# Kernel optimization log

Measured on AMD Instinct MI355X. Metric: run time of the kernel, lower is better.

The kernel has to match this reference:

```python
import jax, jax.numpy as jnp
import numpy as np

N_NODES = 50000
N_FEAT = 128
N_RAND_EDGES = 800000
EPS = 1e-12


def _att_edge_weights(x, row, col, n_node):
    """GNNGuard att_coef: per-edge cosine sim, threshold, zero diagonal,
    row-wise L1 normalize, self-loop weight 1/(deg+1), then exp."""
    # cosine similarity per edge via normalized features (avoids NxN matrix)
    norms = jnp.sqrt(jnp.sum(x * x, axis=1, keepdims=True))
    xn = x / jnp.maximum(norms, EPS)
    sim = jnp.sum(xn[row] * xn[col], axis=1)          # [E]
    sim = jnp.where(sim < 0.1, 0.0, sim)              # threshold
    is_self = (row == col)
    sim = jnp.where(is_self, 0.0, sim)                # remove diagonal (self-sim==1)
    # row-wise L1 normalization (sim >= 0 after threshold)
    rowsum = jax.ops.segment_sum(sim, row, num_segments=n_node)
    rs = rowsum[row]
    sim_norm = jnp.where(rs > 0, sim / jnp.where(rs > 0, rs, 1.0), 0.0)
    # degree = number of nonzero normalized entries per row
    deg = jax.ops.segment_sum((sim_norm != 0).astype(sim.dtype), row,
                              num_segments=n_node)
    lam = 1.0 / (deg + 1.0)                           # self-loop gating weight
    w = jnp.where(is_self, lam[row], sim_norm)
    return jnp.exp(w)


def _gcn_conv(x, row, col, edge_weight, W, b, n_node):
    """GCNConv: h = XW; symmetric-normalized weighted aggregation + bias."""
    h = x @ W                                          # [N, out]
    deg = jax.ops.segment_sum(edge_weight, col, num_segments=n_node)
    dinv = jnp.where(deg > 0, jax.lax.rsqrt(jnp.where(deg > 0, deg, 1.0)), 0.0)
    norm = dinv[row] * edge_weight * dinv[col]         # [E]
    out = jax.ops.segment_sum(norm[:, None] * h[row], col, num_segments=n_node)
    return out + b


def setup_inputs() -> dict:
    key = jax.random.key(0)
    ks = jax.random.split(key, 10)
    x = jax.random.normal(ks[0], (N_NODES, N_FEAT), dtype=jnp.float32)
    # random edges with no self-loops, then append all self-loops
    row = jax.random.randint(ks[1], (N_RAND_EDGES,), 0, N_NODES, dtype=jnp.int32)
    off = jax.random.randint(ks[2], (N_RAND_EDGES,), 1, N_NODES, dtype=jnp.int32)
    col = (row + off) % N_NODES
    loops = jnp.arange(N_NODES, dtype=jnp.int32)
    edge_index = jnp.stack([jnp.concatenate([row, loops]),
                            jnp.concatenate([col, loops])], axis=0)
    s = 1.0 / np.sqrt(N_FEAT)
    W0 = jax.random.normal(ks[3], (N_FEAT, 128), dtype=jnp.float32) * s
    b0 = jnp.zeros((128,), dtype=jnp.float32)
    W1 = jax.random.normal(ks[4], (128, 128), dtype=jnp.float32) * s
    b1 = jnp.zeros((128,), dtype=jnp.float32)
    W2 = jax.random.normal(ks[5], (128, 40), dtype=jnp.float32) * s
    b2 = jnp.zeros((40,), dtype=jnp.float32)
    gate = jax.random.uniform(ks[6], (2,), dtype=jnp.float32)
    return {"x": x, "gate": gate, "W0": W0, "b0": b0, "W1": W1, "b1": b1,
            "W2": W2, "b2": b2, "edge_index": edge_index}


def reference(x, gate, W0, b0, W1, b1, W2, b2, edge_index):
    n = x.shape[0]
    row, col = edge_index[0], edge_index[1]
    Ws = [(W0, b0), (W1, b1), (W2, b2)]
    # layer 0: attention adj from raw features (kept as base adj for gating)
    adj_vals = _att_edge_weights(x, row, col, n)
    h = _gcn_conv(x, row, col, adj_vals, W0, b0, n)
    h = jax.nn.relu(h)
    for i in range(1, 3):
        e_new = _att_edge_weights(h, row, col, n)
        g = gate[i - 1]
        w = g * adj_vals + (1.0 - g) * e_new
        h = _gcn_conv(h, row, col, w, Ws[i][0], Ws[i][1], n)
        if i != 2:
            h = jax.nn.relu(h)
    return jax.nn.log_softmax(h, axis=1)
```

## Files before the change

kernel.cpp:

```cpp
#include <hip/hip_runtime.h>
#include <hip/hip_bf16.h>
#include <math.h>

#define F 128

typedef __attribute__((ext_vector_type(8))) unsigned short ushort8v;

__device__ __forceinline__ float bfu(unsigned short u) {
  return __uint_as_float(((unsigned)u) << 16);
}

__global__ void k_normalize(const float* __restrict__ x, float* __restrict__ xn,
                            __hip_bfloat16* __restrict__ xnb, int N) {
  int wid = (blockIdx.x * blockDim.x + threadIdx.x) >> 6;
  int lane = threadIdx.x & 63;
  if (wid >= N) return;
  const float2* src = (const float2*)(x + (size_t)wid * F);
  float2 v = src[lane];
  float ss = v.x * v.x + v.y * v.y;
#pragma unroll
  for (int m = 32; m >= 1; m >>= 1) ss += __shfl_xor(ss, m);
  float inv = 1.0f / fmaxf(sqrtf(ss), 1e-12f);
  float2 o; o.x = v.x * inv; o.y = v.y * inv;
  ((float2*)(xn + (size_t)wid * F))[lane] = o;
  __hip_bfloat162 ob;
  ob.x = __float2bfloat16(o.x); ob.y = __float2bfloat16(o.y);
  ((__hip_bfloat162*)(xnb + (size_t)wid * F))[lane] = ob;
}

__global__ void k_hist2(const int* __restrict__ row, const int* __restrict__ col,
                        int* __restrict__ cntBoth, int N, int E) {
  int e = blockIdx.x * blockDim.x + threadIdx.x;
  if (e < E) { atomicAdd(cntBoth + col[e], 1); atomicAdd(cntBoth + N + row[e], 1); }
}

__global__ void k_scan1(const int* __restrict__ cnt, int* __restrict__ partial,
                        int* __restrict__ bsum, int M) {
  __shared__ int sm[256];
  int t = threadIdx.x;
  int i = blockIdx.x * 256 + t;
  int val = (i < M) ? cnt[i] : 0;
  sm[t] = val;
  __syncthreads();
  for (int off = 1; off < 256; off <<= 1) {
    int v = (t >= off) ? sm[t - off] : 0;
    __syncthreads();
    sm[t] += v;
    __syncthreads();
  }
  if (i < M) partial[i] = sm[t] - val;
  if (t == 255) bsum[blockIdx.x] = sm[255];
}

__global__ void k_scan2(const int* __restrict__ bsum, int* __restrict__ boffs, int nb) {
  __shared__ int sm[256];
  int t = threadIdx.x;
  int carry = 0;
  for (int base = 0; base < nb; base += 256) {
    int idx = base + t;
    int val = (idx < nb) ? bsum[idx] : 0;
    sm[t] = val;
    __syncthreads();
    for (int off = 1; off < 256; off <<= 1) {
      int v = (t >= off) ? sm[t - off] : 0;
      __syncthreads();
      sm[t] += v;
      __syncthreads();
    }
    if (idx < nb) boffs[idx] = sm[t] - val + carry;
    carry += sm[255];
    __syncthreads();
  }
}

__global__ void k_scan3(const int* __restrict__ partial, const int* __restrict__ boffs,
                        int* __restrict__ offs_c, int* __restrict__ offs_r,
                        int N, int E) {
  int i = blockIdx.x * 256 + threadIdx.x;
  if (i < 2 * N) {
    int v = partial[i] + boffs[i >> 8];
    if (i < N) offs_c[i] = v;
    else offs_r[i - N] = v - E;
  }
  if (i == 0) { offs_c[N] = E; offs_r[N] = E; }
}

__global__ void k_scatter_row(const int* __restrict__ row, const int* __restrict__ offs_r,
                              int* __restrict__ cur_r, int* __restrict__ perm_r, int E) {
  int e = blockIdx.x * blockDim.x + threadIdx.x;
  if (e >= E) return;
  int r = row[e];
  int pos = offs_r[r] + atomicAdd(cur_r + r, 1);
  perm_r[pos] = e;
}

__global__ void k_scatter_col(const int* __restrict__ perm_r, const int* __restrict__ row,
                              const int* __restrict__ col, const int* __restrict__ offs_c,
                              int* __restrict__ cur_c, int* __restrict__ colof_r,
                              int2* __restrict__ pstat, int E) {
  int rp = blockIdx.x * blockDim.x + threadIdx.x;
  if (rp >= E) return;
  int e = perm_r[rp];
  int c = col[e];
  colof_r[rp] = c;
  int pos = offs_c[c] + atomicAdd(cur_c + c, 1);
  int2 rec; rec.x = row[e]; rec.y = rp;
  pstat[pos] = rec;
}

__global__ __launch_bounds__(128) void k_simw(
    const float* __restrict__ xn, const __hip_bfloat16* __restrict__ xnb,
    const int* __restrict__ colof_r, const int* __restrict__ offs_r,
    float* __restrict__ adjr, float* __restrict__ wgr, float* __restrict__ colw,
    const float* __restrict__ gate, int layer) {
  int r = blockIdx.x;
  int t = threadIdx.x;
  int p0 = offs_r[r], p1 = offs_r[r + 1];
  int ne = p1 - p0;
  __shared__ float xr[128];
  __shared__ float sims[320];
  __shared__ int scol[320];
  __shared__ float redv[2];
  __shared__ int redc[2];
  xr[t] = xn[(size_t)r * F + t];
  __syncthreads();
  int g = t >> 4, l = t & 15;
  float4 a0 = *(const float4*)(xr + l * 8);
  float4 a1 = *(const float4*)(xr + l * 8 + 4);
  for (int i = g; i < ne; i += 8) {
    int c = colof_r[p0 + i];
    ushort8v bv = *(const ushort8v*)(xnb + (size_t)c * F + l * 8);
    float s = a0.x * bfu(bv[0]) + a0.y * bfu(bv[1]) + a0.z * bfu(bv[2]) + a0.w * bfu(bv[3])
            + a1.x * bfu(bv[4]) + a1.y * bfu(bv[5]) + a1.z * bfu(bv[6]) + a1.w * bfu(bv[7]);
#pragma unroll
    for (int m = 8; m >= 1; m >>= 1) s += __shfl_xor(s, m);
    bool self = (r == c);
    if (!self && fabsf(s - 0.1f) < 0.02f) {
      const float4* bp = (const float4*)(xn + (size_t)c * F);
      float4 b0 = bp[l * 2], b1 = bp[l * 2 + 1];
      float s2 = a0.x * b0.x + a0.y * b0.y + a0.z * b0.z + a0.w * b0.w
               + a1.x * b1.x + a1.y * b1.y + a1.z * b1.z + a1.w * b1.w;
#pragma unroll
      for (int m = 8; m >= 1; m >>= 1) s2 += __shfl_xor(s2, m);
      s = s2;
    }
    if (l == 0) {
      if (s < 0.1f || self) s = 0.0f;
      sims[i] = s;
      scol[i] = c;
    }
  }
  __syncthreads();
  float v = 0.f; int cn = 0;
  for (int i = t; i < ne; i += 128) {
    float s = sims[i];
    v += s;
    cn += (s > 0.f) ? 1 : 0;
  }
#pragma unroll
  for (int m = 32; m >= 1; m >>= 1) { v += __shfl_xor(v, m); cn += __shfl_xor(cn, m); }
  if ((t & 63) == 0) { redv[t >> 6] = v; redc[t >> 6] = cn; }
  __syncthreads();
  float rs = redv[0] + redv[1];
  int deg = redc[0] + redc[1];
  float lam = 1.0f / (float)(deg + 1);
  float gg = (layer > 0) ? gate[layer - 1] : 0.f;
  for (int i = t; i < ne; i += 128) {
    int c = scol[i];
    float s = sims[i];
    float sn = (rs > 0.f) ? s / rs : 0.f;
    float w = (r == c) ? lam : sn;
    w = expf(w);
    float wc;
    if (layer == 0) { adjr[p0 + i] = w; wc = w; }
    else { wc = gg * adjr[p0 + i] + (1.f - gg) * w; }
    wgr[p0 + i] = wc;
    atomicAdd(colw + c, wc);
  }
}

__global__ __launch_bounds__(256) void k_gemm128(const float* __restrict__ A,
                                                 const float* __restrict__ W,
                                                 __hip_bfloat16* __restrict__ out, int M) {
  __shared__ float As[128][36];
  int t = threadIdx.x;
  int n0 = blockIdx.x * 32;
  for (int i = t; i < 32 * 128; i += 256) {
    int nn = i >> 7, kk = i & 127;
    int gn = n0 + nn;
    As[kk][nn] = (gn < M) ? A[(size_t)gn * 128 + kk] : 0.f;
  }
  __syncthreads();
  int nb = (t >> 6) * 8;
  int j2 = (t & 63) * 2;
  float acc[8][2] = {};
  for (int k = 0; k < 128; ++k) {
    float4 a01 = *(const float4*)&As[k][nb];
    float4 a23 = *(const float4*)&As[k][nb + 4];
    float2 wv = *(const float2*)&W[k * 128 + j2];
    acc[0][0] += a01.x * wv.x; acc[0][1] += a01.x * wv.y;
    acc[1][0] += a01.y * wv.x; acc[1][1] += a01.y * wv.y;
    acc[2][0] += a01.z * wv.x; acc[2][1] += a01.z * wv.y;
    acc[3][0] += a01.w * wv.x; acc[3][1] += a01.w * wv.y;
    acc[4][0] += a23.x * wv.x; acc[4][1] += a23.x * wv.y;
    acc[5][0] += a23.y * wv.x; acc[5][1] += a23.y * wv.y;
    acc[6][0] += a23.z * wv.x; acc[6][1] += a23.z * wv.y;
    acc[7][0] += a23.w * wv.x; acc[7][1] += a23.w * wv.y;
  }
  __hip_bfloat162* o2 = (__hip_bfloat162*)out;
#pragma unroll
  for (int i = 0; i < 8; ++i) {
    int gn = n0 + nb + i;
    if (gn < M) {
      __hip_bfloat162 o;
      o.x = __float2bfloat16(acc[i][0]); o.y = __float2bfloat16(acc[i][1]);
      o2[(size_t)gn * 64 + (j2 >> 1)] = o;
    }
  }
}

__global__ __launch_bounds__(320) void k_gemm40(const float* __restrict__ A,
                                                const float* __restrict__ W,
                                                __hip_bfloat16* __restrict__ out,
                                                int M, int C) {
  __shared__ float As[128][68];
  int t = threadIdx.x;
  int n0 = blockIdx.x * 64;
  for (int i = t; i < 64 * 128; i += 320) {
    int nn = i >> 7, kk = i & 127;
    int gn = n0 + nn;
    As[kk][nn] = (gn < M) ? A[(size_t)gn * 128 + kk] : 0.f;
  }
  __syncthreads();
  int gq = t / 40;
  int jc = t - gq * 40;
  int nb = gq * 8;
  float acc[8] = {};
  for (int k = 0; k < 128; ++k) {
    float4 a01 = *(const float4*)&As[k][nb];
    float4 a23 = *(const float4*)&As[k][nb + 4];
    float wv = W[k * C + jc];
    acc[0] += a01.x * wv; acc[1] += a01.y * wv; acc[2] += a01.z * wv; acc[3] += a01.w * wv;
    acc[4] += a23.x * wv; acc[5] += a23.y * wv; acc[6] += a23.z * wv; acc[7] += a23.w * wv;
  }
#pragma unroll
  for (int i = 0; i < 8; ++i) {
    int gn = n0 + nb + i;
    if (gn < M) out[(size_t)gn * C + jc] = __float2bfloat16(acc[i]);
  }
}

__global__ __launch_bounds__(256) void k_agg_norm(
    const __hip_bfloat162* __restrict__ hWb, const int2* __restrict__ pstat,
    const float* __restrict__ wgr, const float* __restrict__ colw,
    const int* __restrict__ offs_c, const float* __restrict__ bias,
    float* __restrict__ out, float* __restrict__ xn, __hip_bfloat16* __restrict__ xnb,
    int N) {
  int w = threadIdx.x >> 6;
  int t = threadIdx.x & 63;
  int c = blockIdx.x * 4 + w;
  if (c >= N) return;
  int p0 = offs_c[c], p1 = offs_c[c + 1];
  float dcv = colw[c];
  float dic = (dcv > 0.f) ? rsqrtf(dcv) : 0.f;
  float acc0 = bias[2 * t], acc1 = bias[2 * t + 1];
  int p = p0;
  for (; p + 4 <= p1; p += 4) {
    int2 s0 = pstat[p], s1 = pstat[p + 1], s2 = pstat[p + 2], s3 = pstat[p + 3];
    float w0 = wgr[s0.y], w1 = wgr[s1.y], w2 = wgr[s2.y], w3 = wgr[s3.y];
    float d0 = colw[s0.x], d1 = colw[s1.x], d2 = colw[s2.x], d3 = colw[s3.x];
    __hip_bfloat162 h0 = hWb[(size_t)s0.x * 64 + t];
    __hip_bfloat162 h1 = hWb[(size_t)s1.x * 64 + t];
    __hip_bfloat162 h2 = hWb[(size_t)s2.x * 64 + t];
    __hip_bfloat162 h3 = hWb[(size_t)s3.x * 64 + t];
    float n0 = ((d0 > 0.f) ? rsqrtf(d0) : 0.f) * w0 * dic;
    float n1 = ((d1 > 0.f) ? rsqrtf(d1) : 0.f) * w1 * dic;
    float n2 = ((d2 > 0.f) ? rsqrtf(d2) : 0.f) * w2 * dic;
    float n3 = ((d3 > 0.f) ? rsqrtf(d3) : 0.f) * w3 * dic;
    acc0 += n0 * __bfloat162float(h0.x) + n1 * __bfloat162float(h1.x)
          + n2 * __bfloat162float(h2.x) + n3 * __bfloat162float(h3.x);
    acc1 += n0 * __bfloat162float(h0.y) + n1 * __bfloat162float(h1.y)
          + n2 * __bfloat162float(h2.y) + n3 * __bfloat162float(h3.y);
  }
  for (; p < p1; ++p) {
    int2 s0 = pstat[p];
    float w0 = wgr[s0.y];
    float d0 = colw[s0.x];
    __hip_bfloat162 h0 = hWb[(size_t)s0.x * 64 + t];
    float n0 = ((d0 > 0.f) ? rsqrtf(d0) : 0.f) * w0 * dic;
    acc0 += n0 * __bfloat162float(h0.x);
    acc1 += n0 * __bfloat162float(h0.y);
  }
  acc0 = fmaxf(acc0, 0.f); acc1 = fmaxf(acc1, 0.f);
  float2 o; o.x = acc0; o.y = acc1;
  ((float2*)out)[(size_t)c * 64 + t] = o;
  float ss = acc0 * acc0 + acc1 * acc1;
#pragma unroll
  for (int m = 32; m >= 1; m >>= 1) ss += __shfl_xor(ss, m);
  float inv = 1.0f / fmaxf(sqrtf(ss), 1e-12f);
  float2 on; on.x = acc0 * inv; on.y = acc1 * inv;
  ((float2*)xn)[(size_t)c * 64 + t] = on;
  __hip_bfloat162 ob;
  ob.x = __float2bfloat16(on.x); ob.y = __float2bfloat16(on.y);
  ((__hip_bfloat162*)xnb)[(size_t)c * 64 + t] = ob;
}

__global__ __launch_bounds__(256) void k_agg40_lsm(
    const __hip_bfloat16* __restrict__ hW, const int2* __restrict__ pstat,
    const float* __restrict__ wgr, const float* __restrict__ colw,
    const int* __restrict__ offs_c, const float* __restrict__ bias,
    float* __restrict__ out, int C, int N) {
  int w = threadIdx.x >> 6;
  int j = threadIdx.x & 63;
  int c = blockIdx.x * 4 + w;
  if (c >= N) return;
  int p0 = offs_c[c], p1 = offs_c[c + 1];
  float dcv = colw[c];
  float dic = (dcv > 0.f) ? rsqrtf(dcv) : 0.f;
  bool act = j < C;
  int jj = act ? j : 0;
  float acc = act ? bias[jj] : 0.f;
  int p = p0;
  for (; p + 4 <= p1; p += 4) {
    int2 s0 = pstat[p], s1 = pstat[p + 1], s2 = pstat[p + 2], s3 = pstat[p + 3];
    float w0 = wgr[s0.y], w1 = wgr[s1.y], w2 = wgr[s2.y], w3 = wgr[s3.y];
    float d0 = colw[s0.x], d1 = colw[s1.x], d2 = colw[s2.x], d3 = colw[s3.x];
    float h0 = __bfloat162float(hW[(size_t)s0.x * C + jj]);
    float h1 = __bfloat162float(hW[(size_t)s1.x * C + jj]);
    float h2 = __bfloat162float(hW[(size_t)s2.x * C + jj]);
    float h3 = __bfloat162float(hW[(size_t)s3.x * C + jj]);
    acc += ((d0 > 0.f) ? rsqrtf(d0) : 0.f) * w0 * dic * h0
         + ((d1 > 0.f) ? rsqrtf(d1) : 0.f) * w1 * dic * h1
         + ((d2 > 0.f) ? rsqrtf(d2) : 0.f) * w2 * dic * h2
         + ((d3 > 0.f) ? rsqrtf(d3) : 0.f) * w3 * dic * h3;
  }
  for (; p < p1; ++p) {
    int2 s0 = pstat[p];
    float w0 = wgr[s0.y];
    float d0 = colw[s0.x];
    acc += ((d0 > 0.f) ? rsqrtf(d0) : 0.f) * w0 * dic
         * __bfloat162float(hW[(size_t)s0.x * C + jj]);
  }
  if (!act) acc = 0.f;
  float v = act ? acc : -3.0e38f;
#pragma unroll
  for (int m = 32; m >= 1; m >>= 1) v = fmaxf(v, __shfl_xor(v, m));
  float ex = act ? expf(acc - v) : 0.f;
#pragma unroll
  for (int m = 32; m >= 1; m >>= 1) ex += __shfl_xor(ex, m);
  if (act) out[(size_t)c * C + j] = acc - v - logf(ex);
}

extern "C" void kernel_launch(void* const* d_in, const int* in_sizes, int n_in,
                              void* d_out, int out_size, void* d_ws, size_t ws_size,
                              hipStream_t stream) {
  const float* x    = (const float*)d_in[0];
  const float* gate = (const float*)d_in[1];
  const float* W0   = (const float*)d_in[2];
  const float* b0   = (const float*)d_in[3];
  const float* W1   = (const float*)d_in[4];
  const float* b1   = (const float*)d_in[5];
  const float* W2   = (const float*)d_in[6];
  const float* b2   = (const float*)d_in[7];
  const int* eidx   = (const int*)d_in[8];
  int N = in_sizes[0] / 128;
  int E = in_sizes[8] / 2;
  int C = in_sizes[7];
  const int* row = eidx;
  const int* col = eidx + E;

  char* ws = (char*)d_ws;
  size_t off = 0;
  auto alloc = [&](size_t bytes) {
    char* p = ws + off;
    off += (bytes + 255) & ~(size_t)255;
    return p;
  };
  float* xn     = (float*)alloc((size_t)N * 128 * 4);
  __hip_bfloat16* xnb = (__hip_bfloat16*)alloc((size_t)N * 128 * 2);
  float* bufC   = (float*)alloc((size_t)N * 128 * 4);
  __hip_bfloat16* hWb = (__hip_bfloat16*)alloc((size_t)N * 128 * 2);
  float* adjr   = (float*)alloc((size_t)E * 4);
  float* wgr    = (float*)alloc((size_t)E * 4);
  int*   perm_r = (int*)alloc((size_t)E * 4);
  int2*  pstat  = (int2*)alloc((size_t)E * 8);
  int*   colof_r= (int*)alloc((size_t)E * 4);
  int*   offs_c = (int*)alloc((size_t)(N + 1) * 4);
  int*   offs_r = (int*)alloc((size_t)(N + 1) * 4);
  int*   cntB   = (int*)alloc((size_t)N * 4 * 4);
  int*   curB   = cntB + 2 * N;
  int*   partial= (int*)alloc((size_t)N * 4 * 2);
  int*   bsum   = (int*)alloc(2048);
  int*   boffs  = (int*)alloc(2048);
  float* colw   = (float*)alloc((size_t)N * 4);

  int eb  = (E + 255) / 256;
  int nb2 = (2 * N + 255) / 256;
  int nw4 = (N + 3) / 4;

  hipMemsetAsync(cntB, 0, (size_t)N * 4 * 4, stream);
  k_hist2<<<eb, 256, 0, stream>>>(row, col, cntB, N, E);
  k_scan1<<<nb2, 256, 0, stream>>>(cntB, partial, bsum, 2 * N);
  k_scan2<<<1, 256, 0, stream>>>(bsum, boffs, nb2);
  k_scan3<<<nb2, 256, 0, stream>>>(partial, boffs, offs_c, offs_r, N, E);
  k_scatter_row<<<eb, 256, 0, stream>>>(row, offs_r, curB + N, perm_r, E);
  k_scatter_col<<<eb, 256, 0, stream>>>(perm_r, row, col, offs_c, curB,
                                        colof_r, pstat, E);

  for (int layer = 0; layer < 3; ++layer) {
    hipMemsetAsync(colw, 0, (size_t)N * 4, stream);
    if (layer == 0) k_normalize<<<(N + 3) / 4, 256, 0, stream>>>(x, xn, xnb, N);
    k_simw<<<N, 128, 0, stream>>>(xn, xnb, colof_r, offs_r, adjr, wgr, colw, gate, layer);
    const float* hin = (layer == 0) ? x : bufC;
    if (layer < 2) {
      const float* W = (layer == 0) ? W0 : W1;
      const float* b = (layer == 0) ? b0 : b1;
      k_gemm128<<<(N + 31) / 32, 256, 0, stream>>>(hin, W, hWb, N);
      k_agg_norm<<<nw4, 256, 0, stream>>>((const __hip_bfloat162*)hWb, pstat, wgr, colw,
                                          offs_c, b, bufC, xn, xnb, N);
    } else {
      k_gemm40<<<(N + 63) / 64, 320, 0, stream>>>(hin, W2, hWb, N, C);
      k_agg40_lsm<<<nw4, 256, 0, stream>>>(hWb, pstat, wgr, colw, offs_c, b2,
                                           (float*)d_out, C, N);
    }
  }
}
```

Measured before the change: 714.6 us.

## Compute per-edge cosine similarities with MFMA, one wavefront per row

The similarity kernel now gives each row to one wavefront, four rows per block, instead of one 128-thread block per row. Each neighbour's bf16 dot product against the row vector is computed with 16x16x32 bf16 MFMA instructions. The fp32 recheck for similarities near the 0.1 threshold becomes a ballot-driven loop across the whole wave, with the window widened slightly. This aims to cut block-launch and __syncthreads overhead and the scalar dot-product work. In exchange, the MFMA computes a full 16x16 tile when only one column is used, and the threshold fallback is now serialized per wave.

Result: faster. 700.0 us (-2.0%).

```diff
diff --git a/kernel.cpp b/kernel.cpp
--- a/kernel.cpp
+++ b/kernel.cpp
@@ -4,11 +4,8 @@
 
 #define F 128
 
-typedef __attribute__((ext_vector_type(8))) unsigned short ushort8v;
-
-__device__ __forceinline__ float bfu(unsigned short u) {
-  return __uint_as_float(((unsigned)u) << 16);
-}
+typedef __attribute__((ext_vector_type(8))) short bf16x8;
+typedef __attribute__((ext_vector_type(4))) float f32x4;
 
 __global__ void k_normalize(const float* __restrict__ x, float* __restrict__ xn,
                             __hip_bfloat16* __restrict__ xnb, int N) {
@@ -108,72 +105,91 @@
   pstat[pos] = rec;
 }
 
-__global__ __launch_bounds__(128) void k_simw(
+__global__ __launch_bounds__(256) void k_simw(
     const float* __restrict__ xn, const __hip_bfloat16* __restrict__ xnb,
     const int* __restrict__ colof_r, const int* __restrict__ offs_r,
     float* __restrict__ adjr, float* __restrict__ wgr, float* __restrict__ colw,
-    const float* __restrict__ gate, int layer) {
-  int r = blockIdx.x;
-  int t = threadIdx.x;
+    const float* __restrict__ gate, int layer, int N) {
+  int w = threadIdx.x >> 6;
+  int l = threadIdx.x & 63;
+  int r = blockIdx.x * 4 + w;
+  __shared__ float sims[4][320];
+  __shared__ int scol[4][320];
+  if (r >= N) return;
   int p0 = offs_r[r], p1 = offs_r[r + 1];
   int ne = p1 - p0;
-  __shared__ float xr[128];
-  __shared__ float sims[320];
-  __shared__ int scol[320];
-  __shared__ float redv[2];
-  __shared__ int redc[2];
-  xr[t] = xn[(size_t)r * F + t];
-  __syncthreads();
-  int g = t >> 4, l = t & 15;
-  float4 a0 = *(const float4*)(xr + l * 8);
-  float4 a1 = *(const float4*)(xr + l * 8 + 4);
-  for (int i = g; i < ne; i += 8) {
-    int c = colof_r[p0 + i];
-    ushort8v bv = *(const ushort8v*)(xnb + (size_t)c * F + l * 8);
-    float s = a0.x * bfu(bv[0]) + a0.y * bfu(bv[1]) + a0.z * bfu(bv[2]) + a0.w * bfu(bv[3])
-            + a1.x * bfu(bv[4]) + a1.y * bfu(bv[5]) + a1.z * bfu(bv[6]) + a1.w * bfu(bv[7]);
-#pragma unroll
-    for (int m = 8; m >= 1; m >>= 1) s += __shfl_xor(s, m);
-    bool self = (r == c);
-    if (!self && fabsf(s - 0.1f) < 0.02f) {
-      const float4* bp = (const float4*)(xn + (size_t)c * F);
-      float4 b0 = bp[l * 2], b1 = bp[l * 2 + 1];
-      float s2 = a0.x * b0.x + a0.y * b0.y + a0.z * b0.z + a0.w * b0.w
-               + a1.x * b1.x + a1.y * b1.y + a1.z * b1.z + a1.w * b1.w;
-#pragma unroll
-      for (int m = 8; m >= 1; m >>= 1) s2 += __shfl_xor(s2, m);
-      s = s2;
+  int quad = l >> 4;
+  int m = l & 15;
+  int qoff = quad * 8;
+  const __hip_bfloat16* xr = xnb + (size_t)r * F;
+  bf16x8 b0 = *(const bf16x8*)(xr + 0 * 32 + qoff);
+  bf16x8 b1 = *(const bf16x8*)(xr + 1 * 32 + qoff);
+  bf16x8 b2 = *(const bf16x8*)(xr + 2 * 32 + qoff);
+  bf16x8 b3 = *(const bf16x8*)(xr + 3 * 32 + qoff);
+  for (int tb = 0; tb < ne; tb += 16) {
+    int ii = tb + m; if (ii > ne - 1) ii = ne - 1;
+    int cm = colof_r[p0 + ii];
+    if (quad == 0 && tb + m < ne) scol[w][tb + m] = cm;
+    const __hip_bfloat16* xc = xnb + (size_t)cm * F;
+    bf16x8 a0 = *(const bf16x8*)(xc + 0 * 32 + qoff);
+    bf16x8 a1 = *(const bf16x8*)(xc + 1 * 32 + qoff);
+    bf16x8 a2 = *(const bf16x8*)(xc + 2 * 32 + qoff);
+    bf16x8 a3 = *(const bf16x8*)(xc + 3 * 32 + qoff);
+    f32x4 acc = {0.f, 0.f, 0.f, 0.f};
+    acc = __builtin_amdgcn_mfma_f32_16x16x32_bf16(a0, b0, acc, 0, 0, 0);
+    acc = __builtin_amdgcn_mfma_f32_16x16x32_bf16(a1, b1, acc, 0, 0, 0);
+    acc = __builtin_amdgcn_mfma_f32_16x16x32_bf16(a2, b2, acc, 0, 0, 0);
+    acc = __builtin_amdgcn_mfma_f32_16x16x32_bf16(a3, b3, acc, 0, 0, 0);
+    if (m == 0) {
+#pragma unroll
+      for (int reg = 0; reg < 4; ++reg) {
+        int i = tb + quad * 4 + reg;
+        if (i < ne) sims[w][i] = acc[reg];
+      }
     }
-    if (l == 0) {
-      if (s < 0.1f || self) s = 0.0f;
-      sims[i] = s;
-      scol[i] = c;
+  }
+  float vsum = 0.f; int cn = 0;
+  for (int base = 0; base < ne; base += 64) {
+    int i = base + l;
+    bool have = i < ne;
+    float s = have ? sims[w][i] : 0.f;
+    int c = have ? scol[w][i] : r;
+    bool self = (c == r);
+    bool flag = have && !self && fabsf(s - 0.1f) < 0.03f;
+    unsigned long long mask = __ballot(flag);
+    while (mask) {
+      int src = __ffsll(mask) - 1;
+      mask &= mask - 1;
+      int cc = __shfl(c, src);
+      float2 ar = ((const float2*)(xn + (size_t)r * F))[l];
+      float2 bc = ((const float2*)(xn + (size_t)cc * F))[l];
+      float d = ar.x * bc.x + ar.y * bc.y;
+#pragma unroll
+      for (int mm = 32; mm >= 1; mm >>= 1) d += __shfl_xor(d, mm);
+      if (l == src) s = d;
     }
-  }
-  __syncthreads();
-  float v = 0.f; int cn = 0;
-  for (int i = t; i < ne; i += 128) {
-    float s = sims[i];
-    v += s;
+    if (self || s < 0.1f) s = 0.f;
+    if (have) sims[w][i] = s;
+    vsum += s;
     cn += (s > 0.f) ? 1 : 0;
   }
 #pragma unroll
-  for (int m = 32; m >= 1; m >>= 1) { v += __shfl_xor(v, m); cn += __shfl_xor(cn, m); }
-  if ((t & 63) == 0) { redv[t >> 6] = v; redc[t >> 6] = cn; }
-  __syncthreads();
-  float rs = redv[0] + redv[1];
-  int deg = redc[0] + redc[1];
-  float lam = 1.0f / (float)(deg + 1);
+  for (int mm = 32; mm >= 1; mm >>= 1) {
+    vsum += __shfl_xor(vsum, mm);
+    cn += __shfl_xor(cn, mm);
+  }
+  float rs = vsum;
+  float lam = 1.0f / (float)(cn + 1);
   float gg = (layer > 0) ? gate[layer - 1] : 0.f;
-  for (int i = t; i < ne; i += 128) {
-    int c = scol[i];
-    float s = sims[i];
+  for (int i = l; i < ne; i += 64) {
+    int c = scol[w][i];
+    float s = sims[w][i];
     float sn = (rs > 0.f) ? s / rs : 0.f;
-    float w = (r == c) ? lam : sn;
-    w = expf(w);
+    float wv = (c == r) ? lam : sn;
+    wv = expf(wv);
     float wc;
-    if (layer == 0) { adjr[p0 + i] = w; wc = w; }
-    else { wc = gg * adjr[p0 + i] + (1.f - gg) * w; }
+    if (layer == 0) { adjr[p0 + i] = wv; wc = wv; }
+    else { wc = gg * adjr[p0 + i] + (1.f - gg) * wv; }
     wgr[p0 + i] = wc;
     atomicAdd(colw + c, wc);
   }
@@ -410,7 +426,8 @@
   for (int layer = 0; layer < 3; ++layer) {
     hipMemsetAsync(colw, 0, (size_t)N * 4, stream);
     if (layer == 0) k_normalize<<<(N + 3) / 4, 256, 0, stream>>>(x, xn, xnb, N);
-    k_simw<<<N, 128, 0, stream>>>(xn, xnb, colof_r, offs_r, adjr, wgr, colw, gate, layer);
+    k_simw<<<nw4, 256, 0, stream>>>(xn, xnb, colof_r, offs_r, adjr, wgr, colw,
+                                    gate, layer, N);
     const float* hin = (layer == 0) ? x : bufC;
     if (layer < 2) {
       const float* W = (layer == 0) ? W0 : W1;
```
